# Optimization experiments

Measured on AMD Instinct MI355X. Metric: run time of the kernel, lower is better.

Reference implementation:

```python
import jax
jax.config.update("jax_enable_x64", True)
import jax.numpy as jnp
import numpy as np

N = 20000      # nodes per batched graph
E = 320000     # random edges (avg degree 16)
F = 128        # input node features
EMB = 128      # embedding_size
H = 3          # num_heads
G = 128        # graphs in batch (for AvgPooling)
NEG_SLOPE = 0.2  # DGL GATConv attention LeakyReLU slope


def setup_inputs():
    key = jax.random.key(0)
    ks = jax.random.split(key, 40)

    def rn(k, shape):
        return jax.random.normal(k, shape, jnp.float32) * 0.1

    inp = {}
    inp["featsA"] = jax.random.normal(ks[0], (N, F), jnp.float32)
    inp["featsB"] = jax.random.normal(ks[1], (N, F), jnp.float32)
    # edges: random + self-loops so every node has >=1 incoming edge
    for nm, ka, kb in (("A", ks[2], ks[3]), ("B", ks[4], ks[5])):
        src = jnp.concatenate([jax.random.randint(ka, (E,), 0, N, jnp.int32),
                               jnp.arange(N, dtype=jnp.int32)])
        dst = jnp.concatenate([jax.random.randint(kb, (E,), 0, N, jnp.int32),
                               jnp.arange(N, dtype=jnp.int32)])
        inp["src" + nm] = src
        inp["dst" + nm] = dst
        inp["gid" + nm] = ((jnp.arange(N) * G) // N).astype(jnp.int32)

    # per-branch parameters (two independent GATNet_1 branches)
    i = 6
    for nm in ("A", "B"):
        inp["W1" + nm] = rn(ks[i], (F, H * EMB)); i += 1      # gat1A fc
        inp["al1" + nm] = rn(ks[i], (H, EMB)); i += 1          # attn_l
        inp["ar1" + nm] = rn(ks[i], (H, EMB)); i += 1          # attn_r
        inp["b1" + nm] = rn(ks[i], (H * EMB,)); i += 1         # bias
        inp["Wn" + nm] = rn(ks[i], (EMB, H * EMB)); i += 1     # gatn fc
        inp["aln" + nm] = rn(ks[i], (H, EMB)); i += 1
        inp["arn" + nm] = rn(ks[i], (H, EMB)); i += 1
        inp["bn" + nm] = rn(ks[i], (H * EMB,)); i += 1
        inp["Wl" + nm] = rn(ks[i], (H * EMB, EMB)); i += 1     # linear1A
        inp["bl" + nm] = rn(ks[i], (EMB,)); i += 1
    inp["Wo"] = rn(ks[i], (2 * EMB, 1)); i += 1                # DoubleNet.output
    inp["bo"] = rn(ks[i], (1,))
    return inp


def gat_layer(feat, src, dst, W, al, ar, b):
    # DGL GATConv (eval mode: feat_drop/attn_drop are identity)
    n = feat.shape[0]
    z = (feat @ W).reshape(n, H, -1)                     # [N,H,D]
    el = (z * al[None]).sum(-1)                          # [N,H]
    er = (z * ar[None]).sum(-1)
    e = jax.nn.leaky_relu(el[src] + er[dst], NEG_SLOPE)  # [E,H]
    # edge softmax over incoming edges of each dst node
    m = jax.ops.segment_max(e, dst, num_segments=n)
    a = jnp.exp(e - m[dst])
    den = jax.ops.segment_sum(a, dst, num_segments=n)
    a = a / den[dst]
    out = jax.ops.segment_sum(a[:, :, None] * z[src], dst, num_segments=n)  # [N,H,D]
    return out + b.reshape(1, H, -1)


def branch(feat, src, dst, gid, W1, al1, ar1, b1, Wn, aln, arn, bn, Wl, bl):
    n = feat.shape[0]
    x = gat_layer(feat, src, dst, W1, al1, ar1, b1).reshape(n, -1)
    x = x @ Wl + bl
    for _ in range(2):  # two applications of the SAME gatn/linear1A weights
        x = gat_layer(x, src, dst, Wn, aln, arn, bn).reshape(n, -1)
        x = x @ Wl + bl
        # nn.LeakyReLU(True): negative_slope == 1.0 -> identity (faithful)
    s = jax.ops.segment_sum(x, gid, num_segments=G)
    cnt = jax.ops.segment_sum(jnp.ones((n,), x.dtype), gid, num_segments=G)
    return s / cnt[:, None]


def reference(featsA, featsB, srcA, dstA, gidA, srcB, dstB, gidB,
              W1A, al1A, ar1A, b1A, WnA, alnA, arnA, bnA, WlA, blA,
              W1B, al1B, ar1B, b1B, WnB, alnB, arnB, bnB, WlB, blB,
              Wo, bo):
    x = branch(featsA, srcA, dstA, gidA, W1A, al1A, ar1A, b1A,
               WnA, alnA, arnA, bnA, WlA, blA)
    y = branch(featsB, srcB, dstB, gidB, W1B, al1B, ar1B, b1B,
               WnB, alnB, arnB, bnB, WlB, blB)
    cat = jnp.concatenate([x, y], axis=1)                # [G, 2*EMB]
    z = cat @ Wo + bo
    return z.astype(jnp.float64)                         # .double()
```

## Files before the change

kernel.cpp:

```cpp
#include <hip/hip_runtime.h>
#include <hip/hip_bf16.h>
#include <math.h>

#define NN  20000
#define FF  128
#define EMB 128
#define HH  3
#define GG  128
#define HD  384
#define ELL 64

typedef __attribute__((ext_vector_type(8))) short short8;
typedef __attribute__((ext_vector_type(4))) float f32x4;

__device__ inline float bf2f(unsigned int u){
  union{unsigned int i; float f;} v; v.i = u<<16; return v.f;
}
__device__ inline unsigned short f2bf(float f){
  union{unsigned int i; float f;} v; v.f = f;
  unsigned r = v.i + 0x7FFFu + ((v.i>>16)&1u);
  return (unsigned short)(r>>16);
}

__global__ __launch_bounds__(256) void prep(
    const float* __restrict__ W1A, const float* __restrict__ al1A, const float* __restrict__ ar1A,
    const float* __restrict__ WnA, const float* __restrict__ alnA, const float* __restrict__ arnA,
    const float* __restrict__ W1B, const float* __restrict__ al1B, const float* __restrict__ ar1B,
    const float* __restrict__ WnB, const float* __restrict__ alnB, const float* __restrict__ arnB,
    const float* __restrict__ WlA, const float* __restrict__ blA,
    const float* __restrict__ WlB, const float* __restrict__ blB,
    const float* __restrict__ b1A, const float* __restrict__ bnA,
    const float* __restrict__ b1B, const float* __restrict__ bnB,
    unsigned short* __restrict__ MT, float* __restrict__ V, float* __restrict__ cbuf,
    const int* __restrict__ srcA, const int* __restrict__ dstA,
    const int* __restrict__ srcB, const int* __restrict__ dstB,
    int* __restrict__ cntA, int* __restrict__ cntB,
    int* __restrict__ slotA, int* __restrict__ slotB, int ne, int nbE){
  __shared__ float As[16][65];
  __shared__ float Bs[16][65];
  int bid = blockIdx.x;
  int wv = threadIdx.x >> 6, lane = threadIdx.x & 63;

  if (bid < 48){
    int mh = bid >> 2;
    int mat = mh / 3, h = mh - mat*3;
    int tile = bid & 3; int tp = (tile>>1)*64, tq = (tile&1)*64;
    const float* W  = (mat==0)?W1A:(mat==1)?WnA:(mat==2)?W1B:WnB;
    const float* Wl = (mat<2)? WlA : WlB;
    int tid = threadIdx.x;
    int tq4 = (tid&15)<<2, tp4 = (tid>>4)<<2;
    int sd = tid >> 4, sc4 = (tid&15)<<2;
    float acc[4][4] = {};
    for (int d0=0; d0<128; d0+=16){
      #pragma unroll
      for (int i=0;i<4;i++)
        As[sd][sc4+i] = W[(size_t)(tp+sc4+i)*HD + h*128 + d0+sd];
      float4 b4 = *(const float4*)&Wl[(size_t)(h*128+d0+sd)*128 + tq + sc4];
      Bs[sd][sc4+0]=b4.x; Bs[sd][sc4+1]=b4.y; Bs[sd][sc4+2]=b4.z; Bs[sd][sc4+3]=b4.w;
      __syncthreads();
      #pragma unroll
      for (int k=0;k<16;k++){
        float a[4], bb[4];
        #pragma unroll
        for (int i=0;i<4;i++) a[i] = As[k][tp4+i];
        #pragma unroll
        for (int jq=0;jq<4;jq++) bb[jq] = Bs[k][tq4+jq];
        #pragma unroll
        for (int i=0;i<4;i++)
          #pragma unroll
          for (int jq=0;jq<4;jq++)
            acc[i][jq] += a[i]*bb[jq];
      }
      __syncthreads();
    }
    #pragma unroll
    for (int jq=0;jq<4;jq++)
      #pragma unroll
      for (int i=0;i<4;i++)
        MT[(size_t)mat*49152 + (size_t)(tq+tq4+jq)*HD + h*128 + tp+tp4+i] = f2bf(acc[i][jq]);
  } else if (bid < 816){
    int idx = (bid-48)*4 + wv;
    int mat = idx / 768; int rem = idx - mat*768;
    int j = rem >> 7, k = rem & 127;
    int h = (j >= 3) ? j-3 : j; bool isr = j >= 3;
    const float* W = (mat==0)?W1A:(mat==1)?WnA:(mat==2)?W1B:WnB;
    const float* a;
    if (mat==0)      a = isr?ar1A:al1A;
    else if (mat==1) a = isr?arnA:alnA;
    else if (mat==2) a = isr?ar1B:al1B;
    else             a = isr?arnB:alnB;
    float s = W[(size_t)k*HD + h*128 + lane]      * a[h*128 + lane]
            + W[(size_t)k*HD + h*128 + 64 + lane] * a[h*128 + 64 + lane];
    #pragma unroll
    for (int o=32;o;o>>=1) s += __shfl_xor(s,o);
    if (lane == 0) V[(size_t)mat*768 + j*128 + k] = s;
  } else if (bid < 944){
    int idx = (bid-816)*4 + wv;
    int mat = idx >> 7, q = idx & 127;
    const float* bvec = (mat==0)?b1A:(mat==1)?bnA:(mat==2)?b1B:bnB;
    const float* Wl = (mat<2)?WlA:WlB;
    const float* bl = (mat<2)?blA:blB;
    float s = 0.f;
    #pragma unroll
    for (int r=0;r<6;r++){
      int j = r*64 + lane;
      s += bvec[j]*Wl[(size_t)j*128 + q];
    }
    #pragma unroll
    for (int o=32;o;o>>=1) s += __shfl_xor(s,o);
    if (lane == 0) cbuf[mat*128 + q] = s + bl[q];
  } else {
    int bb = bid - 944; int isB = bb >= nbE;
    const int* src = isB ? srcB : srcA;
    const int* dst = isB ? dstB : dstA;
    int* cnt  = isB ? cntB : cntA;
    int* slot = isB ? slotB : slotA;
    int i = (isB ? bb-nbE : bb)*256 + threadIdx.x;
    if (i < ne){
      int d = dst[i];
      int p = atomicAdd(&cnt[d], 1);
      if (p < ELL) slot[d*ELL + p] = src[i];
    }
  }
}

__global__ __launch_bounds__(256) void conv_elr1(
    const float* __restrict__ fA, const float* __restrict__ fB,
    unsigned short* __restrict__ XA, unsigned short* __restrict__ XB,
    const float* __restrict__ V,
    float* __restrict__ el, float* __restrict__ er){
  int gn = blockIdx.x*4 + (threadIdx.x>>6);
  int lane = threadIdx.x & 63;
  int b = gn >= NN; int n = b ? gn - NN : gn;
  const float* feats = b ? fB : fA;
  unsigned short* X = b ? XB : XA;
  const float* Vb = V + (size_t)(b*2 + 0)*768;
  float2 xv = ((const float2*)feats)[(size_t)n*64 + lane];
  ((unsigned*)(X + (size_t)n*EMB))[lane] =
      (unsigned)f2bf(xv.x) | ((unsigned)f2bf(xv.y)<<16);
  float x0 = bf2f((unsigned)f2bf(xv.x)), x1 = bf2f((unsigned)f2bf(xv.y));
  int c0 = 2*lane;
  #pragma unroll
  for (int j=0;j<6;j++){
    float v = x0*Vb[j*128 + c0] + x1*Vb[j*128 + c0 + 1];
    #pragma unroll
    for (int o=32;o;o>>=1) v += __shfl_xor(v,o);
    if (lane == 0){
      if (j < 3) el[(size_t)gn*3 + j] = v;
      else       er[(size_t)gn*3 + (j-3)] = v;
    }
  }
}

#define GAS __attribute__((address_space(1)))
#define LAS __attribute__((address_space(3)))
__device__ inline void gll16(void* lds, const void* g){
  __builtin_amdgcn_global_load_lds((const GAS unsigned int*)g,
                                   (LAS unsigned int*)lds, 16, 0, 0);
}

__global__ __launch_bounds__(256) void gemm_mfma(
    const unsigned short* __restrict__ A0, const unsigned short* __restrict__ A1,
    const unsigned short* __restrict__ BT0, const unsigned short* __restrict__ BT1,
    const float* __restrict__ bias0, const float* __restrict__ bias1,
    unsigned short* __restrict__ C0, unsigned short* __restrict__ C1,
    int M, int N, int K){
  const unsigned short* A  = blockIdx.z ? A1 : A0;
  const unsigned short* BT = blockIdx.z ? BT1 : BT0;
  const float* bias        = blockIdx.z ? bias1 : bias0;
  unsigned short* C        = blockIdx.z ? C1 : C0;

  __shared__ __align__(16) unsigned short As[4][128][8];
  __shared__ __align__(16) unsigned short Bs[4][64][8];
  int tid = threadIdx.x;
  int w = tid >> 6, l = tid & 63;
  int wm = w >> 1, wn = w & 1;
  int l16 = l & 15, lq = l >> 4;
  int blockRow = blockIdx.y * 128;
  int blockCol = blockIdx.x * 64;
  f32x4 acc[4][2] = {};

  int arow0 = blockRow + l;       if (arow0 >= M) arow0 = M-1;
  int arow1 = blockRow + 64 + l;  if (arow1 >= M) arow1 = M-1;
  const unsigned short* aptr0 = A + (size_t)arow0*K + w*8;
  const unsigned short* aptr1 = A + (size_t)arow1*K + w*8;
  const unsigned short* bptr  = BT + (size_t)(blockCol + l)*K + w*8;
  unsigned short* alds0 = &As[w][0][0];
  unsigned short* alds1 = &As[w][64][0];
  unsigned short* blds  = &Bs[w][0][0];

  for (int k0 = 0; k0 < K; k0 += 32){
    gll16(alds0, aptr0 + k0);
    gll16(alds1, aptr1 + k0);
    gll16(blds,  bptr  + k0);
    __syncthreads();
    short8 af[4], bfr[2];
    #pragma unroll
    for (int mi=0;mi<4;mi++)
      af[mi] = *(const short8*)&As[lq][wm*64 + mi*16 + l16][0];
    #pragma unroll
    for (int ni=0;ni<2;ni++)
      bfr[ni] = *(const short8*)&Bs[lq][wn*32 + ni*16 + l16][0];
    #pragma unroll
    for (int mi=0;mi<4;mi++)
      #pragma unroll
      for (int ni=0;ni<2;ni++)
        acc[mi][ni] = __builtin_amdgcn_mfma_f32_16x16x32_bf16(af[mi], bfr[ni], acc[mi][ni], 0, 0, 0);
    __syncthreads();
  }

  #pragma unroll
  for (int ni=0;ni<2;ni++){
    int col = blockCol + wn*32 + ni*16 + l16;
    float bv = bias ? bias[col] : 0.f;
    #pragma unroll
    for (int mi=0;mi<4;mi++){
      #pragma unroll
      for (int r=0;r<4;r++){
        int row = blockRow + wm*64 + mi*16 + lq*4 + r;
        if (row < M)
          C[(size_t)row*N + col] = f2bf(acc[mi][ni][r] + bv);
      }
    }
  }
}

__global__ __launch_bounds__(256) void elr2(
    const unsigned short* __restrict__ X0, const unsigned short* __restrict__ X1,
    const float* __restrict__ V,
    float* __restrict__ el, float* __restrict__ er){
  int gn = blockIdx.x*4 + (threadIdx.x>>6);
  int lane = threadIdx.x & 63;
  int b = gn >= NN; int n = b ? gn - NN : gn;
  const unsigned short* X = b ? X1 : X0;
  const float* Vb = V + (size_t)(b*2 + 1)*768;
  unsigned u = ((const unsigned*)(X + (size_t)n*EMB))[lane];
  float xlo = bf2f(u & 0xFFFFu), xhi = bf2f(u>>16);
  int c0 = 2*lane;
  #pragma unroll
  for (int j=0;j<6;j++){
    float v = xlo*Vb[j*128 + c0] + xhi*Vb[j*128 + c0 + 1];
    #pragma unroll
    for (int o=32;o;o>>=1) v += __shfl_xor(v,o);
    if (lane == 0){
      if (j < 3) el[(size_t)gn*3 + j] = v;
      else       er[(size_t)gn*3 + (j-3)] = v;
    }
  }
}

__global__ __launch_bounds__(256) void gat_agg(
    const unsigned short* __restrict__ X0, const unsigned short* __restrict__ X1,
    const float* __restrict__ el, const float* __restrict__ er,
    const int* __restrict__ cntA, const int* __restrict__ cntB,
    const int* __restrict__ slotA, const int* __restrict__ slotB,
    unsigned short* __restrict__ U0, unsigned short* __restrict__ U1){
  int wv = threadIdx.x >> 6, lane = threadIdx.x & 63;
  int gn = blockIdx.x*4 + wv;
  int b = gn >= NN; int n = b ? gn - NN : gn;
  const unsigned short* X = b ? X1 : X0;
  const int* cnt  = b ? cntB : cntA;
  const int* slot = b ? slotB : slotA;
  unsigned short* U = b ? U1 : U0;
  const float* elb = el + (size_t)b*NN*3;

  int deg = cnt[n]; if (deg > ELL) deg = ELL;
  float er0 = er[(size_t)gn*3+0], er1 = er[(size_t)gn*3+1], er2 = er[(size_t)gn*3+2];

  int s = 0;
  float e0 = -3e38f, e1 = -3e38f, e2 = -3e38f;
  if (lane < deg){
    s = slot[n*ELL + lane];
    float t0 = elb[s*3+0]+er0; e0 = t0>0.f ? t0 : 0.2f*t0;
    float t1 = elb[s*3+1]+er1; e1 = t1>0.f ? t1 : 0.2f*t1;
    float t2 = elb[s*3+2]+er2; e2 = t2>0.f ? t2 : 0.2f*t2;
  }
  float m0 = e0, m1 = e1, m2 = e2;
  #pragma unroll
  for (int o=32;o;o>>=1){
    m0 = fmaxf(m0, __shfl_xor(m0,o));
    m1 = fmaxf(m1, __shfl_xor(m1,o));
    m2 = fmaxf(m2, __shfl_xor(m2,o));
  }
  float p0 = __expf(e0-m0), p1 = __expf(e1-m1), p2 = __expf(e2-m2);
  float d0 = p0, d1 = p1, d2 = p2;
  #pragma unroll
  for (int o=32;o;o>>=1){
    d0 += __shfl_xor(d0,o); d1 += __shfl_xor(d1,o); d2 += __shfl_xor(d2,o);
  }
  float a0 = p0/d0, a1 = p1/d1, a2 = p2/d2;
  int a0i = __float_as_int(a0), a1i = __float_as_int(a1), a2i = __float_as_int(a2);

  float ax0=0.f,ay0=0.f,ax1=0.f,ay1=0.f,ax2=0.f,ay2=0.f;
  const unsigned* Xw = (const unsigned*)X;
  int npad = (deg + 3) & ~3;
  for (int e = 0; e < npad; e += 4){
    #pragma unroll
    for (int u2 = 0; u2 < 4; u2++){
      int idx = e + u2;
      int sl = __builtin_amdgcn_readlane(s, idx);
      float w0 = __int_as_float(__builtin_amdgcn_readlane(a0i, idx));
      float w1 = __int_as_float(__builtin_amdgcn_readlane(a1i, idx));
      float w2 = __int_as_float(__builtin_amdgcn_readlane(a2i, idx));
      unsigned xu = Xw[(size_t)sl*64 + lane];
      float lo = bf2f(xu & 0xFFFFu), hi = bf2f(xu >> 16);
      ax0 += w0*lo; ay0 += w0*hi;
      ax1 += w1*lo; ay1 += w1*hi;
      ax2 += w2*lo; ay2 += w2*hi;
    }
  }

  unsigned* op = (unsigned*)(U + (size_t)n*HD);
  op[lane]      = (unsigned)f2bf(ax0) | ((unsigned)f2bf(ay0)<<16);
  op[64+lane]   = (unsigned)f2bf(ax1) | ((unsigned)f2bf(ay1)<<16);
  op[128+lane]  = (unsigned)f2bf(ax2) | ((unsigned)f2bf(ay2)<<16);
}

__device__ inline int lbound(const int* __restrict__ a, int n, int v){
  int lo = 0, hi = n;
  while (lo < hi){ int mid = (lo+hi)>>1; if (a[mid] < v) lo = mid+1; else hi = mid; }
  return lo;
}

__global__ __launch_bounds__(512) void pool_kernel(
    const unsigned short* __restrict__ X0, const unsigned short* __restrict__ X1,
    const int* __restrict__ gidA, const int* __restrict__ gidB,
    float* __restrict__ ps){
  int bg = blockIdx.x;
  int b = bg >= GG; int g = b ? bg-GG : bg;
  const unsigned short* X = b ? X1 : X0;
  const int* gid = b ? gidB : gidA;
  int lo = lbound(gid, NN, g), hi = lbound(gid, NN, g+1);
  int t = threadIdx.x;
  int rl = t >> 6, c2 = t & 63;
  float ax = 0.f, ay = 0.f;
  for (int n = lo + rl; n < hi; n += 8){
    unsigned u = ((const unsigned*)(X + (size_t)n*EMB))[c2];
    ax += bf2f(u & 0xFFFFu); ay += bf2f(u >> 16);
  }
  __shared__ float sh[8][128];
  sh[rl][2*c2] = ax; sh[rl][2*c2+1] = ay;
  __syncthreads();
  if (t < 128){
    float s = 0.f;
    #pragma unroll
    for (int r=0;r<8;r++) s += sh[r][t];
    ps[(size_t)bg*EMB + t] = s / (float)(hi - lo);
  }
}

__global__ void final_kernel(const float* __restrict__ ps,
                             const float* __restrict__ Wo, const float* __restrict__ bo,
                             float* __restrict__ out){
  int g = blockIdx.x*4 + (threadIdx.x>>6);
  int lane = threadIdx.x & 63;
  if (g >= GG) return;
  float v = 0.f;
  #pragma unroll
  for (int r=0;r<4;r++){
    int k = r*64 + lane;
    float cv = (k < EMB) ? ps[(size_t)g*EMB + k]
                         : ps[(size_t)(GG + g)*EMB + (k-EMB)];
    v += cv * Wo[k];
  }
  #pragma unroll
  for (int o=32;o;o>>=1) v += __shfl_xor(v,o);
  if (lane == 0) out[g] = v + bo[0];
}

extern "C" void kernel_launch(void* const* d_in, const int* in_sizes, int n_in,
                              void* d_out, int out_size, void* d_ws, size_t ws_size,
                              hipStream_t stream){
  const float* featsA = (const float*)d_in[0];
  const float* featsB = (const float*)d_in[1];
  const int* srcA = (const int*)d_in[2];
  const int* dstA = (const int*)d_in[3];
  const int* gidA = (const int*)d_in[4];
  const int* srcB = (const int*)d_in[5];
  const int* dstB = (const int*)d_in[6];
  const int* gidB = (const int*)d_in[7];
  const int EE = in_sizes[2];
  const float* P[2][10];
  for (int b=0;b<2;b++)
    for (int j=0;j<10;j++)
      P[b][j] = (const float*)d_in[8 + b*10 + j];
  const float* Wo = (const float*)d_in[28];
  const float* bo = (const float*)d_in[29];
  float* out = (float*)d_out;

  char* ws = (char*)d_ws;
  size_t o = 0;
  auto alloc = [&](size_t bytes)->char*{
    char* p = ws + o; o += (bytes + 255) & ~(size_t)255; return p;
  };
  unsigned short* bufU[2] = {(unsigned short*)alloc((size_t)NN*HD*2),
                             (unsigned short*)alloc((size_t)NN*HD*2)};
  unsigned short* bufX[2] = {(unsigned short*)alloc((size_t)NN*EMB*2),
                             (unsigned short*)alloc((size_t)NN*EMB*2)};
  unsigned short* fbf[2] = {(unsigned short*)alloc((size_t)NN*FF*2),
                            (unsigned short*)alloc((size_t)NN*FF*2)};
  unsigned short* MT = (unsigned short*)alloc((size_t)4*49152*2);
  float* V    = (float*)alloc((size_t)4*768*4);
  float* cbuf = (float*)alloc((size_t)4*128*4);
  float* el   = (float*)alloc((size_t)2*NN*3*4);
  float* er   = (float*)alloc((size_t)2*NN*3*4);
  int*   cntA = (int*)alloc((size_t)2*NN*4);
  int*   cntB = cntA + NN;
  int*   slotA= (int*)alloc((size_t)NN*ELL*4);
  int*   slotB= (int*)alloc((size_t)NN*ELL*4);
  float* ps   = (float*)alloc((size_t)2*GG*EMB*4);

  const int nbE = (EE + 255)/256;
  const int nwB = 2*NN/4;
  dim3 gWL(EMB/64, (NN+127)/128, 2);

  hipMemsetAsync(cntA, 0, (size_t)2*NN*4, stream);
  prep<<<944 + 2*nbE, 256, 0, stream>>>(
      P[0][0],P[0][1],P[0][2], P[0][4],P[0][5],P[0][6],
      P[1][0],P[1][1],P[1][2], P[1][4],P[1][5],P[1][6],
      P[0][8],P[0][9], P[1][8],P[1][9],
      P[0][3],P[0][7], P[1][3],P[1][7],
      MT, V, cbuf,
      srcA,dstA, srcB,dstB, cntA,cntB, slotA,slotB, EE, nbE);
  conv_elr1<<<nwB,256,0,stream>>>(featsA, featsB, fbf[0], fbf[1], V, el, er);

  gat_agg<<<nwB,256,0,stream>>>(fbf[0], fbf[1], el, er, cntA,cntB, slotA,slotB,
                                bufU[0], bufU[1]);
  gemm_mfma<<<gWL,256,0,stream>>>(bufU[0],bufU[1], MT + 0*49152, MT + 2*49152,
                                  cbuf + 0*128, cbuf + 2*128,
                                  bufX[0],bufX[1], NN, EMB, HD);

  for (int it=0; it<2; it++){
    elr2<<<nwB,256,0,stream>>>(bufX[0], bufX[1], V, el, er);
    gat_agg<<<nwB,256,0,stream>>>(bufX[0], bufX[1], el, er, cntA,cntB, slotA,slotB,
                                  bufU[0], bufU[1]);
    gemm_mfma<<<gWL,256,0,stream>>>(bufU[0],bufU[1], MT + 1*49152, MT + 3*49152,
                                    cbuf + 1*128, cbuf + 3*128,
                                    bufX[0],bufX[1], NN, EMB, HD);
  }

  pool_kernel<<<2*GG,512,0,stream>>>(bufX[0],bufX[1], gidA,gidB, ps);
  final_kernel<<<(GG+3)/4,256,0,stream>>>(ps, Wo, bo, out);
}
```

Measured before the change: 286.7 us.

## Narrow edge slots to 16-bit, pad el/er to float4, retile weight-fold prep

Stores source indices in the ELL slot table as 16-bit values, which fits because N is 20000, and halves that table's traffic. The per-node attention logits el/er are padded from 3 to 4 floats so each gathered source logit is one aligned float4 load. The prep weight-fold GEMM now uses a 32-deep K tile with coalesced float4 loads and a transposed LDS write. The bf16 unpack in aggregation uses plain shift and mask. The added cost is padding memory, and the 16-bit indices only work while N stays below 65536.

```diff
diff --git a/kernel.cpp b/kernel.cpp
--- a/kernel.cpp
+++ b/kernel.cpp
@@ -35,9 +35,9 @@
     const int* __restrict__ srcA, const int* __restrict__ dstA,
     const int* __restrict__ srcB, const int* __restrict__ dstB,
     int* __restrict__ cntA, int* __restrict__ cntB,
-    int* __restrict__ slotA, int* __restrict__ slotB, int ne, int nbE){
-  __shared__ float As[16][65];
-  __shared__ float Bs[16][65];
+    unsigned short* __restrict__ slotA, unsigned short* __restrict__ slotB, int ne, int nbE){
+  __shared__ float As[32][65];
+  __shared__ float Bs[32][65];
   int bid = blockIdx.x;
   int wv = threadIdx.x >> 6, lane = threadIdx.x & 63;
 
@@ -49,17 +49,25 @@
     const float* Wl = (mat<2)? WlA : WlB;
     int tid = threadIdx.x;
     int tq4 = (tid&15)<<2, tp4 = (tid>>4)<<2;
-    int sd = tid >> 4, sc4 = (tid&15)<<2;
     float acc[4][4] = {};
-    for (int d0=0; d0<128; d0+=16){
-      #pragma unroll
-      for (int i=0;i<4;i++)
-        As[sd][sc4+i] = W[(size_t)(tp+sc4+i)*HD + h*128 + d0+sd];
-      float4 b4 = *(const float4*)&Wl[(size_t)(h*128+d0+sd)*128 + tq + sc4];
-      Bs[sd][sc4+0]=b4.x; Bs[sd][sc4+1]=b4.y; Bs[sd][sc4+2]=b4.z; Bs[sd][sc4+3]=b4.w;
+    for (int d0=0; d0<128; d0+=32){
+      {
+        int p = tid>>3, dd = (tid&7)<<2;
+        float4 a0 = *(const float4*)&W[(size_t)(tp+p)*HD + h*128 + d0 + dd];
+        float4 a1 = *(const float4*)&W[(size_t)(tp+p+32)*HD + h*128 + d0 + dd];
+        As[dd+0][p]=a0.x; As[dd+1][p]=a0.y; As[dd+2][p]=a0.z; As[dd+3][p]=a0.w;
+        As[dd+0][p+32]=a1.x; As[dd+1][p+32]=a1.y; As[dd+2][p+32]=a1.z; As[dd+3][p+32]=a1.w;
+      }
+      {
+        int dd = tid>>4, q4 = (tid&15)<<2;
+        float4 b0 = *(const float4*)&Wl[(size_t)(h*128+d0+dd)*128 + tq + q4];
+        float4 b1 = *(const float4*)&Wl[(size_t)(h*128+d0+dd+16)*128 + tq + q4];
+        Bs[dd][q4+0]=b0.x; Bs[dd][q4+1]=b0.y; Bs[dd][q4+2]=b0.z; Bs[dd][q4+3]=b0.w;
+        Bs[dd+16][q4+0]=b1.x; Bs[dd+16][q4+1]=b1.y; Bs[dd+16][q4+2]=b1.z; Bs[dd+16][q4+3]=b1.w;
+      }
       __syncthreads();
       #pragma unroll
-      for (int k=0;k<16;k++){
+      for (int k=0;k<32;k++){
         float a[4], bb[4];
         #pragma unroll
         for (int i=0;i<4;i++) a[i] = As[k][tp4+i];
@@ -114,12 +122,12 @@
     const int* src = isB ? srcB : srcA;
     const int* dst = isB ? dstB : dstA;
     int* cnt  = isB ? cntB : cntA;
-    int* slot = isB ? slotB : slotA;
+    unsigned short* slot = isB ? slotB : slotA;
     int i = (isB ? bb-nbE : bb)*256 + threadIdx.x;
     if (i < ne){
       int d = dst[i];
       int p = atomicAdd(&cnt[d], 1);
-      if (p < ELL) slot[d*ELL + p] = src[i];
+      if (p < ELL) slot[d*ELL + p] = (unsigned short)src[i];
     }
   }
 }
@@ -146,8 +154,8 @@
     #pragma unroll
     for (int o=32;o;o>>=1) v += __shfl_xor(v,o);
     if (lane == 0){
-      if (j < 3) el[(size_t)gn*3 + j] = v;
-      else       er[(size_t)gn*3 + (j-3)] = v;
+      if (j < 3) el[(size_t)gn*4 + j] = v;
+      else       er[(size_t)gn*4 + (j-3)] = v;
     }
   }
 }
@@ -243,8 +251,8 @@
     #pragma unroll
     for (int o=32;o;o>>=1) v += __shfl_xor(v,o);
     if (lane == 0){
-      if (j < 3) el[(size_t)gn*3 + j] = v;
-      else       er[(size_t)gn*3 + (j-3)] = v;
+      if (j < 3) el[(size_t)gn*4 + j] = v;
+      else       er[(size_t)gn*4 + (j-3)] = v;
     }
   }
 }
@@ -253,27 +261,28 @@
     const unsigned short* __restrict__ X0, const unsigned short* __restrict__ X1,
     const float* __restrict__ el, const float* __restrict__ er,
     const int* __restrict__ cntA, const int* __restrict__ cntB,
-    const int* __restrict__ slotA, const int* __restrict__ slotB,
+    const unsigned short* __restrict__ slotA, const unsigned short* __restrict__ slotB,
     unsigned short* __restrict__ U0, unsigned short* __restrict__ U1){
   int wv = threadIdx.x >> 6, lane = threadIdx.x & 63;
   int gn = blockIdx.x*4 + wv;
   int b = gn >= NN; int n = b ? gn - NN : gn;
   const unsigned short* X = b ? X1 : X0;
   const int* cnt  = b ? cntB : cntA;
-  const int* slot = b ? slotB : slotA;
+  const unsigned short* slot = b ? slotB : slotA;
   unsigned short* U = b ? U1 : U0;
-  const float* elb = el + (size_t)b*NN*3;
+  const float* elb = el + (size_t)b*NN*4;
 
   int deg = cnt[n]; if (deg > ELL) deg = ELL;
-  float er0 = er[(size_t)gn*3+0], er1 = er[(size_t)gn*3+1], er2 = er[(size_t)gn*3+2];
+  float er0 = er[(size_t)gn*4+0], er1 = er[(size_t)gn*4+1], er2 = er[(size_t)gn*4+2];
 
   int s = 0;
   float e0 = -3e38f, e1 = -3e38f, e2 = -3e38f;
   if (lane < deg){
-    s = slot[n*ELL + lane];
-    float t0 = elb[s*3+0]+er0; e0 = t0>0.f ? t0 : 0.2f*t0;
-    float t1 = elb[s*3+1]+er1; e1 = t1>0.f ? t1 : 0.2f*t1;
-    float t2 = elb[s*3+2]+er2; e2 = t2>0.f ? t2 : 0.2f*t2;
+    s = (int)slot[n*ELL + lane];
+    float4 ev = *(const float4*)(elb + (size_t)s*4);
+    float t0 = ev.x+er0; e0 = t0>0.f ? t0 : 0.2f*t0;
+    float t1 = ev.y+er1; e1 = t1>0.f ? t1 : 0.2f*t1;
+    float t2 = ev.z+er2; e2 = t2>0.f ? t2 : 0.2f*t2;
   }
   float m0 = e0, m1 = e1, m2 = e2;
   #pragma unroll
@@ -303,7 +312,8 @@
       float w1 = __int_as_float(__builtin_amdgcn_readlane(a1i, idx));
       float w2 = __int_as_float(__builtin_amdgcn_readlane(a2i, idx));
       unsigned xu = Xw[(size_t)sl*64 + lane];
-      float lo = bf2f(xu & 0xFFFFu), hi = bf2f(xu >> 16);
+      float lo = __int_as_float(xu << 16);
+      float hi = __int_as_float(xu & 0xffff0000u);
       ax0 += w0*lo; ay0 += w0*hi;
       ax1 += w1*lo; ay1 += w1*hi;
       ax2 += w2*lo; ay2 += w2*hi;
@@ -402,12 +412,12 @@
   unsigned short* MT = (unsigned short*)alloc((size_t)4*49152*2);
   float* V    = (float*)alloc((size_t)4*768*4);
   float* cbuf = (float*)alloc((size_t)4*128*4);
-  float* el   = (float*)alloc((size_t)2*NN*3*4);
-  float* er   = (float*)alloc((size_t)2*NN*3*4);
+  float* el   = (float*)alloc((size_t)2*NN*4*4);
+  float* er   = (float*)alloc((size_t)2*NN*4*4);
   int*   cntA = (int*)alloc((size_t)2*NN*4);
   int*   cntB = cntA + NN;
-  int*   slotA= (int*)alloc((size_t)NN*ELL*4);
-  int*   slotB= (int*)alloc((size_t)NN*ELL*4);
+  unsigned short* slotA = (unsigned short*)alloc((size_t)NN*ELL*2);
+  unsigned short* slotB = (unsigned short*)alloc((size_t)NN*ELL*2);
   float* ps   = (float*)alloc((size_t)2*GG*EMB*4);
 
   const int nbE = (EE + 255)/256;
```

Result: no change. 291.8 us (+1.8%).
